# Optimization experiments

Measured on AMD Instinct MI355X. Metric: run time of the kernel, lower is better.

Reference implementation:

```python
import jax, jax.numpy as jnp
import numpy as np

D = 1024
H = 16
HD = D // H
L = 2048
B = 1
MLP = 8192
ROPE_BASE = 10000.0
LN_EPS = 1e-5


def layer_norm(x):
    mu = jnp.mean(x, axis=-1, keepdims=True)
    var = jnp.var(x, axis=-1, keepdims=True)
    return (x - mu) / jnp.sqrt(var + LN_EPS)


def rope(x):
    # x: [B, H, L, HD]; non-traditional (rotate-half / NeoX style)
    half = HD // 2
    inv_freq = 1.0 / (ROPE_BASE ** (jnp.arange(0, half, dtype=jnp.float32) / half))
    pos = jnp.arange(x.shape[2], dtype=jnp.float32)
    ang = pos[:, None] * inv_freq[None, :]            # [L, half]
    cos, sin = jnp.cos(ang), jnp.sin(ang)
    x1, x2 = x[..., :half], x[..., half:]
    return jnp.concatenate([x1 * cos - x2 * sin, x2 * cos + x1 * sin], axis=-1).astype(x.dtype)


def setup_inputs() -> dict:
    key = jax.random.key(0)
    ks = jax.random.split(key, 5)
    x = jax.random.normal(ks[0], (B, L, D), dtype=jnp.float32)
    # causal additive mask
    neg = jnp.finfo(jnp.float32).min
    mask = jnp.where(jnp.tril(jnp.ones((L, L), dtype=bool)), 0.0, neg).astype(jnp.float32)
    W_attn = jax.random.normal(ks[1], (3 * D, D), dtype=jnp.float32) * (D ** -0.5)
    W_out = jax.random.normal(ks[2], (D, D), dtype=jnp.float32) * (D ** -0.5)
    W_ffp = jax.random.normal(ks[3], (MLP, D), dtype=jnp.float32) * (D ** -0.5)
    W_ffo = jax.random.normal(ks[4], (D, MLP // 2), dtype=jnp.float32) * ((MLP // 2) ** -0.5)
    return {"x": x, "mask": mask, "W_attn": W_attn, "W_out": W_out, "W_ffp": W_ffp, "W_ffo": W_ffo}


def block(x, mask, W_attn, W_out, W_ffp, W_ffo):
    b, l, d = x.shape
    scale = HD ** -0.5
    # attention branch
    xn = layer_norm(x)
    qkv = xn @ W_attn.T                                    # [B, L, 3D]
    q, k, v = jnp.split(qkv, 3, axis=-1)
    q = q.reshape(b, l, H, HD).transpose(0, 2, 1, 3)       # [B, H, L, HD]
    k = k.reshape(b, l, H, HD).transpose(0, 2, 1, 3)
    v = v.reshape(b, l, H, HD).transpose(0, 2, 1, 3)
    q = rope(q)
    k = rope(k)
    scores = jnp.einsum('bhqd,bhkd->bhqk', q * scale, k)   # [B, H, L, L]
    scores = scores + mask
    probs = jax.nn.softmax(scores.astype(jnp.float32), axis=-1).astype(scores.dtype)
    attn = jnp.einsum('bhqk,bhkd->bhqd', probs, v)
    attn = attn.transpose(0, 2, 1, 3).reshape(b, l, d)
    r = attn @ W_out.T
    h = x + r
    # SwiGLU MLP branch: split ff_proj output, swiglu(x2, x1) = silu(x2) * x1
    g = layer_norm(h) @ W_ffp.T                            # [B, L, MLP]
    x1, x2 = jnp.split(g, 2, axis=-1)
    mlp = (jax.nn.silu(x2) * x1) @ W_ffo.T
    return h + mlp


def reference(x, mask, W_attn, W_out, W_ffp, W_ffo):
    return block(x, mask, W_attn, W_out, W_ffp, W_ffo)
```

## Files before the change

### kernel.cpp

```cpp
#include <hip/hip_runtime.h>
#include <math.h>

#define DMODEL 1024
#define NHEAD  16
#define HDIM   64
#define SEQ    2048
#define MLPD   8192
#define HALF_MLP 4096
static constexpr float LN_EPS_C = 1e-5f;
#define NEG_BIG (-1e30f)
#define SM_SHIFT 16.0f

typedef short bf16x8 __attribute__((ext_vector_type(8)));
typedef float f32x4  __attribute__((ext_vector_type(4)));

__device__ __forceinline__ unsigned short f2b(float f) {
    unsigned int u = __float_as_uint(f);
    u = (u + 0x7FFFu + ((u >> 16) & 1u)) >> 16;
    return (unsigned short)u;
}
__device__ __forceinline__ float b2f(unsigned short h) {
    return __uint_as_float((unsigned int)h << 16);
}

__device__ __forceinline__ void async_copy16(const unsigned short* g, unsigned short* l) {
    __builtin_amdgcn_global_load_lds(
        (const __attribute__((address_space(1))) unsigned int*)(g),
        (__attribute__((address_space(3))) unsigned int*)(l),
        16, 0, 0);
}

__global__ void prep_all(const float* __restrict__ x,
                         const float* __restrict__ W_attn, const float* __restrict__ W_out,
                         const float* __restrict__ W_ffp,  const float* __restrict__ W_ffo,
                         unsigned short* __restrict__ xnb, float2* __restrict__ ct,
                         unsigned short* __restrict__ oa, unsigned short* __restrict__ ob,
                         unsigned short* __restrict__ oc, unsigned short* __restrict__ od) {
    const int bid = blockIdx.x;
    const int tid = threadIdx.x;
    if (bid < SEQ) {
        __shared__ float rs[256], rs2[256];
        float4 v = *(const float4*)(x + (size_t)bid * DMODEL + tid * 4);
        rs[tid]  = v.x + v.y + v.z + v.w;
        rs2[tid] = v.x * v.x + v.y * v.y + v.z * v.z + v.w * v.w;
        __syncthreads();
        for (int off = 128; off > 0; off >>= 1) {
            if (tid < off) { rs[tid] += rs[tid + off]; rs2[tid] += rs2[tid + off]; }
            __syncthreads();
        }
        float mu  = rs[0] * (1.0f / DMODEL);
        float var = rs2[0] * (1.0f / DMODEL) - mu * mu;
        float inv = rsqrtf(var + LN_EPS_C);
        ushort4 o;
        o.x = f2b((v.x - mu) * inv); o.y = f2b((v.y - mu) * inv);
        o.z = f2b((v.z - mu) * inv); o.w = f2b((v.w - mu) * inv);
        *(ushort4*)(xnb + (size_t)bid * DMODEL + tid * 4) = o;
    } else if (bid < SEQ + 256) {
        int idx = (bid - SEQ) * 256 + tid;
        int pos = idx >> 5, p = idx & 31;
        float invf = powf(10000.0f, -(float)p / 32.0f);
        float ang = (float)pos * invf;
        ct[idx] = make_float2(cosf(ang), sinf(ang));
    } else {
        const int n1 = 3 * DMODEL * DMODEL;
        const int n2 = n1 + DMODEL * DMODEL;
        const int n3 = n2 + MLPD * DMODEL;
        int i = ((bid - SEQ - 256) * 256 + tid) * 4;
        const float* src; unsigned short* dst; int off;
        if (i < n1)      { src = W_attn; dst = oa; off = i; }
        else if (i < n2) { src = W_out;  dst = ob; off = i - n1; }
        else if (i < n3) {
            src = W_ffp; off = i - n2;
            int row = off >> 10, col = off & 1023;
            int rp  = (row < HALF_MLP) ? (2 * row) : (2 * (row - HALF_MLP) + 1);
            float4 v = *(const float4*)(src + off);
            ushort4 o;
            o.x = f2b(v.x); o.y = f2b(v.y); o.z = f2b(v.z); o.w = f2b(v.w);
            *(ushort4*)(oc + ((size_t)rp << 10) + col) = o;
            return;
        }
        else             { src = W_ffo; dst = od; off = i - n3; }
        float4 v = *(const float4*)(src + off);
        ushort4 o;
        o.x = f2b(v.x); o.y = f2b(v.y); o.z = f2b(v.z); o.w = f2b(v.w);
        *(ushort4*)(dst + off) = o;
    }
}

__global__ void ln_red2(const float* __restrict__ p0, const float* __restrict__ p1,
                        const float* __restrict__ x, float* __restrict__ h,
                        unsigned short* __restrict__ xnb) {
    const int row = blockIdx.x;
    const int tid = threadIdx.x;
    __shared__ float rs[256], rs2[256];
    const size_t base = (size_t)row * DMODEL + tid * 4;
    float4 a = *(const float4*)(p0 + base);
    float4 b = *(const float4*)(p1 + base);
    float4 r = *(const float4*)(x + base);
    float4 v = { a.x + b.x + r.x, a.y + b.y + r.y, a.z + b.z + r.z, a.w + b.w + r.w };
    *(float4*)(h + base) = v;
    rs[tid]  = v.x + v.y + v.z + v.w;
    rs2[tid] = v.x * v.x + v.y * v.y + v.z * v.z + v.w * v.w;
    __syncthreads();
    for (int off = 128; off > 0; off >>= 1) {
        if (tid < off) { rs[tid] += rs[tid + off]; rs2[tid] += rs2[tid + off]; }
        __syncthreads();
    }
    float mu  = rs[0] * (1.0f / DMODEL);
    float var = rs2[0] * (1.0f / DMODEL) - mu * mu;
    float inv = rsqrtf(var + LN_EPS_C);
    ushort4 o;
    o.x = f2b((v.x - mu) * inv); o.y = f2b((v.y - mu) * inv);
    o.z = f2b((v.z - mu) * inv); o.w = f2b((v.w - mu) * inv);
    *(ushort4*)(xnb + base) = o;
}

__global__ __launch_bounds__(256)
void gemm_qkv(const unsigned short* __restrict__ A, const unsigned short* __restrict__ B,
              const float2* __restrict__ ct,
              unsigned short* __restrict__ Qp, unsigned short* __restrict__ Kp,
              unsigned short* __restrict__ Vt) {
    __shared__ unsigned short As[128 * 32];
    __shared__ unsigned short Bs[128 * 32];
    __shared__ unsigned short St[4][16][72];
    const int tid  = threadIdx.x;
    const int lane = tid & 63;
    const int w    = tid >> 6;
    const int wm   = w >> 1;
    const int wn   = w & 1;
    const int m0   = blockIdx.y * 128;
    const int n0   = blockIdx.x * 128;

    f32x4 acc[4][4] = {};

    const int srow = lane >> 2;
    const int scol = (lane & 3) * 8;
    const unsigned short* Abase = A + (size_t)(m0 + w * 32 + srow) * DMODEL + scol;
    const unsigned short* Bbase = B + (size_t)(n0 + w * 32 + srow) * DMODEL + scol;
    unsigned short* AsW = &As[(w * 32) * 32];
    unsigned short* BsW = &Bs[(w * 32) * 32];

    const int fr = lane & 15;
    const int fk = (lane >> 4) * 8;

    for (int k0 = 0; k0 < DMODEL; k0 += 32) {
        async_copy16(Abase + k0,               AsW);
        async_copy16(Abase + k0 + 16 * DMODEL, AsW + 16 * 32);
        async_copy16(Bbase + k0,               BsW);
        async_copy16(Bbase + k0 + 16 * DMODEL, BsW + 16 * 32);
        __syncthreads();

        bf16x8 af[4], bfr[4];
#pragma unroll
        for (int i = 0; i < 4; ++i)
            af[i] = *(const bf16x8*)(&As[(wm * 64 + i * 16 + fr) * 32 + fk]);
#pragma unroll
        for (int j = 0; j < 4; ++j)
            bfr[j] = *(const bf16x8*)(&Bs[(wn * 64 + j * 16 + fr) * 32 + fk]);
#pragma unroll
        for (int i = 0; i < 4; ++i)
#pragma unroll
            for (int j = 0; j < 4; ++j)
                acc[i][j] = __builtin_amdgcn_mfma_f32_16x16x32_bf16(af[i], bfr[j], acc[i][j], 0, 0, 0);
        __syncthreads();
    }

    const int erow   = (lane >> 4) * 4;
    const int ecol   = lane & 15;
    const int region = blockIdx.x >> 3;
    const int head   = ((n0 + wn * 64) >> 6) & 15;

    if (region == 2) {
        const int sbase = m0 + wm * 64;
        const int dl = lane >> 3;
        const int ch = (lane & 7) * 8;
#pragma unroll
        for (int j = 0; j < 4; ++j) {
#pragma unroll
            for (int i = 0; i < 4; ++i) {
                ushort4 o;
                o.x = f2b(acc[i][j][0]); o.y = f2b(acc[i][j][1]);
                o.z = f2b(acc[i][j][2]); o.w = f2b(acc[i][j][3]);
                *(ushort4*)&St[w][ecol][i * 16 + erow] = o;
            }
#pragma unroll
            for (int p = 0; p < 2; ++p) {
                const int dd = p * 8 + dl;
                bf16x8 v = *(const bf16x8*)&St[w][dd][ch];
                *(bf16x8*)(Vt + ((size_t)head * HDIM + j * 16 + dd) * SEQ + sbase + ch) = v;
            }
        }
    } else {
        unsigned short* P = region ? Kp : Qp;
        const float scale = region ? 1.0f : 0.125f;
        unsigned short* qb = &St[w][erow][0];
#pragma unroll
        for (int i = 0; i < 4; ++i) {
#pragma unroll
            for (int r = 0; r < 4; ++r) {
                const int rowg = m0 + wm * 64 + i * 16 + erow + r;
                const float2* crow = ct + (size_t)rowg * 32;
#pragma unroll
                for (int jj = 0; jj < 2; ++jj) {
                    const float2 cs = crow[jj * 16 + ecol];
                    const float x1 = acc[i][jj][r];
                    const float x2 = acc[i][jj + 2][r];
                    qb[jj * 16 + ecol]      = f2b((x1 * cs.x - x2 * cs.y) * scale);
                    qb[jj * 16 + ecol + 32] = f2b((x2 * cs.x + x1 * cs.y) * scale);
                }
                ushort4 o = *(const ushort4*)&qb[ecol * 4];
                *(ushort4*)(P + ((size_t)head * SEQ + rowg) * HDIM + ecol * 4) = o;
            }
        }
    }
}

__global__ __launch_bounds__(256)
void gemm_mfma_sk(const unsigned short* __restrict__ A, const unsigned short* __restrict__ B,
                  float* __restrict__ P, int Ksub, int lda, int ldb, int ldc) {
    __shared__ unsigned short As[128 * 32];
    __shared__ unsigned short Bs[128 * 32];
    const int tid  = threadIdx.x;
    const int lane = tid & 63;
    const int w    = tid >> 6;
    const int wm   = w >> 1;
    const int wn   = w & 1;
    const int m0   = blockIdx.y * 128;
    const int n0   = blockIdx.x * 128;
    const int kb   = blockIdx.z * Ksub;

    f32x4 acc[4][4] = {};

    const int srow = lane >> 2;
    const int scol = (lane & 3) * 8;
    const unsigned short* Abase = A + (size_t)(m0 + w * 32 + srow) * lda + scol + kb;
    const unsigned short* Bbase = B + (size_t)(n0 + w * 32 + srow) * ldb + scol + kb;
    unsigned short* AsW = &As[(w * 32) * 32];
    unsigned short* BsW = &Bs[(w * 32) * 32];

    const int fr = lane & 15;
    const int fk = (lane >> 4) * 8;

    for (int k0 = 0; k0 < Ksub; k0 += 32) {
        async_copy16(Abase + k0,            AsW);
        async_copy16(Abase + k0 + 16 * lda, AsW + 16 * 32);
        async_copy16(Bbase + k0,            BsW);
        async_copy16(Bbase + k0 + 16 * (size_t)ldb, BsW + 16 * 32);
        __syncthreads();

        bf16x8 af[4], bfr[4];
#pragma unroll
        for (int i = 0; i < 4; ++i)
            af[i] = *(const bf16x8*)(&As[(wm * 64 + i * 16 + fr) * 32 + fk]);
#pragma unroll
        for (int j = 0; j < 4; ++j)
            bfr[j] = *(const bf16x8*)(&Bs[(wn * 64 + j * 16 + fr) * 32 + fk]);
#pragma unroll
        for (int i = 0; i < 4; ++i)
#pragma unroll
            for (int j = 0; j < 4; ++j)
                acc[i][j] = __builtin_amdgcn_mfma_f32_16x16x32_bf16(af[i], bfr[j], acc[i][j], 0, 0, 0);
        __syncthreads();
    }

    float* Pp = P + (size_t)blockIdx.z * SEQ * ldc;
    const int erow = (lane >> 4) * 4;
    const int ecol = lane & 15;
#pragma unroll
    for (int i = 0; i < 4; ++i)
#pragma unroll
        for (int j = 0; j < 4; ++j) {
            const int colg = n0 + wn * 64 + j * 16 + ecol;
#pragma unroll
            for (int r = 0; r < 4; ++r) {
                const int rowg = m0 + wm * 64 + i * 16 + erow + r;
                Pp[(size_t)rowg * ldc + colg] = acc[i][j][r];
            }
        }
}

__global__ void reduce4_kernel(const float* __restrict__ p0, const float* __restrict__ p1,
                               const float* __restrict__ p2, const float* __restrict__ p3,
                               const float* __restrict__ res, float* __restrict__ out) {
    int i = (blockIdx.x * blockDim.x + threadIdx.x) * 4;
    float4 a = *(const float4*)(p0 + i);
    float4 b = *(const float4*)(p1 + i);
    float4 c = *(const float4*)(p2 + i);
    float4 d = *(const float4*)(p3 + i);
    float4 r = *(const float4*)(res + i);
    float4 o = { a.x + b.x + c.x + d.x + r.x, a.y + b.y + c.y + d.y + r.y,
                 a.z + b.z + c.z + d.z + r.z, a.w + b.w + c.w + d.w + r.w };
    *(float4*)(out + i) = o;
}

#define STW 40
__global__ __launch_bounds__(256)
void gemm_ffp_silu(const unsigned short* __restrict__ A, const unsigned short* __restrict__ B,
                   unsigned short* __restrict__ gact) {
    __shared__ unsigned short As[128 * 32];
    __shared__ unsigned short Bs[128 * 32];
    __shared__ unsigned short St[4][64][STW];
    const int tid  = threadIdx.x;
    const int lane = tid & 63;
    const int w    = tid >> 6;
    const int wm   = w >> 1;
    const int wn   = w & 1;
    const int m0   = blockIdx.y * 128;
    const int n0   = blockIdx.x * 128;

    f32x4 acc[4][4] = {};

    const int srow = lane >> 2;
    const int scol = (lane & 3) * 8;
    const unsigned short* Abase = A + (size_t)(m0 + w * 32 + srow) * DMODEL + scol;
    const unsigned short* Bbase = B + (size_t)(n0 + w * 32 + srow) * DMODEL + scol;
    unsigned short* AsW = &As[(w * 32) * 32];
    unsigned short* BsW = &Bs[(w * 32) * 32];

    const int fr = lane & 15;
    const int fk = (lane >> 4) * 8;

    for (int k0 = 0; k0 < DMODEL; k0 += 32) {
        async_copy16(Abase + k0,               AsW);
        async_copy16(Abase + k0 + 16 * DMODEL, AsW + 16 * 32);
        async_copy16(Bbase + k0,               BsW);
        async_copy16(Bbase + k0 + 16 * DMODEL, BsW + 16 * 32);
        __syncthreads();

        bf16x8 af[4], bfr[4];
#pragma unroll
        for (int i = 0; i < 4; ++i)
            af[i] = *(const bf16x8*)(&As[(wm * 64 + i * 16 + fr) * 32 + fk]);
#pragma unroll
        for (int j = 0; j < 4; ++j)
            bfr[j] = *(const bf16x8*)(&Bs[(wn * 64 + j * 16 + fr) * 32 + fk]);
#pragma unroll
        for (int i = 0; i < 4; ++i)
#pragma unroll
            for (int j = 0; j < 4; ++j)
                acc[i][j] = __builtin_amdgcn_mfma_f32_16x16x32_bf16(af[i], bfr[j], acc[i][j], 0, 0, 0);
        __syncthreads();
    }

    const int erow = (lane >> 4) * 4;
    const int ecol = lane & 15;
    const bool evn = (ecol & 1) == 0;
#pragma unroll
    for (int i = 0; i < 4; ++i)
#pragma unroll
        for (int j = 0; j < 4; ++j)
#pragma unroll
            for (int r = 0; r < 4; ++r) {
                float own = acc[i][j][r];
                float oth = __shfl_xor(own, 1);
                if (evn) {
                    float sil = oth / (1.0f + __expf(-oth));
                    St[w][i * 16 + erow + r][j * 8 + (ecol >> 1)] = f2b(sil * own);
                }
            }
    {
        const int rowg = m0 + wm * 64 + lane;
        unsigned short* dst = gact + (size_t)rowg * HALF_MLP + (n0 >> 1) + wn * 32;
        bf16x8 v0 = *(const bf16x8*)&St[w][lane][0];
        bf16x8 v1 = *(const bf16x8*)&St[w][lane][8];
        bf16x8 v2 = *(const bf16x8*)&St[w][lane][16];
        bf16x8 v3 = *(const bf16x8*)&St[w][lane][24];
        *(bf16x8*)(dst + 0)  = v0;
        *(bf16x8*)(dst + 8)  = v1;
        *(bf16x8*)(dst + 16) = v2;
        *(bf16x8*)(dst + 24) = v3;
    }
}

__global__ __launch_bounds__(256)
void fattn_blk(const unsigned short* __restrict__ Qp,
               const unsigned short* __restrict__ Kp,
               const unsigned short* __restrict__ Vt,
               unsigned short* __restrict__ out) {
    __shared__ unsigned short Ks[2][64][64];
    __shared__ unsigned short Vs[2][64][64];
    __shared__ unsigned short Ps[4][16][72];
    const int tid  = threadIdx.x;
    const int lane = tid & 63;
    const int w    = tid >> 6;
    const int fr   = lane & 15;
    const int quad = lane >> 4;

    const int f    = blockIdx.x;
    const int head = ((f & 7) << 1) | ((f >> 3) & 1);
    const int ub   = f >> 4;
    const int qb   = (ub & 1) ? (31 - (ub >> 1)) : (ub >> 1);
    const int m0   = qb * 64 + w * 16;

    const unsigned short* Qg = Qp + (size_t)head * SEQ * HDIM;
    const unsigned short* Kg = Kp + (size_t)head * SEQ * HDIM;
    const unsigned short* Vg = Vt + (size_t)head * HDIM * SEQ;

    const int rA = (w << 3) + (lane >> 3);
    const int cg = ((lane & 7) ^ ((lane >> 3) & 7)) << 3;

    bf16x8 qf[2];
#pragma unroll
    for (int kk = 0; kk < 2; ++kk)
        qf[kk] = *(const bf16x8*)(Qg + (size_t)(m0 + fr) * HDIM + kk * 32 + quad * 8);

    bf16x8 ones;
#pragma unroll
    for (int e = 0; e < 8; ++e) ones[e] = (short)0x3F80;

    f32x4 accO[4] = {};
    f32x4 accL = {};

    const int ntiles = qb + 1;

    {
        const unsigned short* gk = Kg + (size_t)rA * HDIM + cg;
        unsigned short* dk = &Ks[0][w << 3][0];
        async_copy16(gk, dk);
        async_copy16(gk + 32 * HDIM, dk + 32 * 64);
        const unsigned short* gv = Vg + (size_t)rA * SEQ + cg;
        unsigned short* dv = &Vs[0][w << 3][0];
        async_copy16(gv, dv);
        async_copy16(gv + 32 * SEQ, dv + 32 * 64);
    }
    __syncthreads();

    int cur = 0;
    for (int t = 0; t < ntiles; ++t) {
        if (t + 1 < ntiles) {
            const int j1 = (t + 1) * 64;
            const unsigned short* gk = Kg + (size_t)(j1 + rA) * HDIM + cg;
            unsigned short* dk = &Ks[cur ^ 1][w << 3][0];
            async_copy16(gk, dk);
            async_copy16(gk + 32 * HDIM, dk + 32 * 64);
            const unsigned short* gv = Vg + (size_t)rA * SEQ + j1 + cg;
            unsigned short* dv = &Vs[cur ^ 1][w << 3][0];
            async_copy16(gv, dv);
            async_copy16(gv + 32 * SEQ, dv + 32 * 64);
        }

        const int j0 = t * 64;
        f32x4 accS[4] = {};
#pragma unroll
        for (int kk = 0; kk < 2; ++kk) {
#pragma unroll
            for (int j = 0; j < 4; ++j) {
                bf16x8 kf = *(const bf16x8*)
                    &Ks[cur][j * 16 + fr][(((kk << 2) + quad) ^ (fr & 7)) << 3];
                accS[j] = __builtin_amdgcn_mfma_f32_16x16x32_bf16(qf[kk], kf, accS[j], 0, 0, 0);
            }
        }

        if (t == ntiles - 1) {
#pragma unroll
            for (int j = 0; j < 4; ++j)
#pragma unroll
                for (int r = 0; r < 4; ++r)
                    if (j0 + j * 16 + fr > m0 + quad * 4 + r) accS[j][r] = NEG_BIG;
        }

#pragma unroll
        for (int j = 0; j < 4; ++j)
#pragma unroll
            for (int r = 0; r < 4; ++r)
                Ps[w][quad * 4 + r][j * 16 + fr] = f2b(__expf(accS[j][r] - SM_SHIFT));

#pragma unroll
        for (int kk = 0; kk < 2; ++kk) {
            bf16x8 pf = *(const bf16x8*)&Ps[w][fr][kk * 32 + quad * 8];
            accL = __builtin_amdgcn_mfma_f32_16x16x32_bf16(pf, ones, accL, 0, 0, 0);
#pragma unroll
            for (int j = 0; j < 4; ++j) {
                bf16x8 vf = *(const bf16x8*)
                    &Vs[cur][j * 16 + fr][(((kk << 2) + quad) ^ (fr & 7)) << 3];
                accO[j] = __builtin_amdgcn_mfma_f32_16x16x32_bf16(pf, vf, accO[j], 0, 0, 0);
            }
        }

        __syncthreads();
        cur ^= 1;
    }

#pragma unroll
    for (int r = 0; r < 4; ++r) {
        const float inv = 1.0f / accL[r];
        const int qrow = m0 + quad * 4 + r;
#pragma unroll
        for (int j = 0; j < 4; ++j)
            out[(size_t)qrow * DMODEL + head * HDIM + j * 16 + fr] = f2b(accO[j][r] * inv);
    }
}

extern "C" void kernel_launch(void* const* d_in, const int* in_sizes, int n_in,
                              void* d_out, int out_size, void* d_ws, size_t ws_size,
                              hipStream_t stream) {
    const float* x      = (const float*)d_in[0];
    const float* W_attn = (const float*)d_in[2];
    const float* W_out  = (const float*)d_in[3];
    const float* W_ffp  = (const float*)d_in[4];
    const float* W_ffo  = (const float*)d_in[5];
    float* out = (float*)d_out;

    char* wsb = (char*)d_ws;
    unsigned short* wb_attn = (unsigned short*)(wsb);
    unsigned short* wb_out  = (unsigned short*)(wsb + (6u  << 20));
    unsigned short* wb_ffp  = (unsigned short*)(wsb + (8u  << 20));
    unsigned short* wb_ffo  = (unsigned short*)(wsb + (24u << 20));
    float*          h       = (float*)(wsb + (32u << 20));
    unsigned short* xnb     = (unsigned short*)(wsb + (40u << 20));
    unsigned short* attnb   = (unsigned short*)(wsb + (44u << 20));
    unsigned short* gact    = (unsigned short*)(wsb + (48u << 20));
    unsigned short* Qp      = (unsigned short*)(wsb + (64u << 20));
    unsigned short* Kp      = (unsigned short*)(wsb + (68u << 20));
    unsigned short* Vt      = (unsigned short*)(wsb + (72u << 20));
    float*          wout_p  = (float*)(wsb + (76u << 20));
    float2*         ct      = (float2*)(wsb + (92u << 20));
    float*          ffo_p   = (float*)(wsb + (64u << 20));

    {
        int f2b_blocks = (3 * DMODEL * DMODEL + DMODEL * DMODEL + MLPD * DMODEL
                          + DMODEL * HALF_MLP) / 4 / 256;
        prep_all<<<SEQ + 256 + f2b_blocks, 256, 0, stream>>>(
            x, W_attn, W_out, W_ffp, W_ffo, xnb, ct,
            wb_attn, wb_out, wb_ffp, wb_ffo);
    }

    gemm_qkv<<<dim3(3 * DMODEL / 128, SEQ / 128), 256, 0, stream>>>(
        xnb, wb_attn, ct, Qp, Kp, Vt);

    fattn_blk<<<512, 256, 0, stream>>>(Qp, Kp, Vt, attnb);

    gemm_mfma_sk<<<dim3(DMODEL / 128, SEQ / 128, 2), 256, 0, stream>>>(
        attnb, wb_out, wout_p, DMODEL / 2, DMODEL, DMODEL, DMODEL);

    ln_red2<<<SEQ, 256, 0, stream>>>(wout_p, wout_p + (size_t)SEQ * DMODEL, x, h, xnb);

    gemm_ffp_silu<<<dim3(MLPD / 128, SEQ / 128), 256, 0, stream>>>(
        xnb, wb_ffp, gact);

    gemm_mfma_sk<<<dim3(DMODEL / 128, SEQ / 128, 4), 256, 0, stream>>>(
        gact, wb_ffo, ffo_p, HALF_MLP / 4, HALF_MLP, HALF_MLP, DMODEL);

    reduce4_kernel<<<SEQ * DMODEL / 4 / 256, 256, 0, stream>>>(
        ffo_p, ffo_p + (size_t)SEQ * DMODEL, ffo_p + 2 * (size_t)SEQ * DMODEL,
        ffo_p + 3 * (size_t)SEQ * DMODEL, h, out);
}
```

Before: 310.9 us.

## Rewrite FFP SwiGLU GEMM with 256x256 tiles and multi-stage async pipeline

Replaces the 128x128, 256-thread FFP+SiLU GEMM with a 512-thread kernel computing 256x256 output tiles. Global-to-LDS copies rotate through four buffers, prefetching two k-steps ahead, with explicit vmcnt waits and a single barrier per iteration. It also adds an XOR swizzle on LDS chunks to avoid bank conflicts, a block-index remap for L2 locality, and raised wave priority around the MFMA loop. The aim is to hide load latency and raise arithmetic intensity, at the cost of 128KB of LDS per block and higher register pressure from the larger accumulator, which limits occupancy.

```diff
diff --git a/kernel.cpp b/kernel.cpp
--- a/kernel.cpp
+++ b/kernel.cpp
@@ -293,60 +293,93 @@
     *(float4*)(out + i) = o;
 }
 
-#define STW 40
-__global__ __launch_bounds__(256)
-void gemm_ffp_silu(const unsigned short* __restrict__ A, const unsigned short* __restrict__ B,
-                   unsigned short* __restrict__ gact) {
-    __shared__ unsigned short As[128 * 32];
-    __shared__ unsigned short Bs[128 * 32];
-    __shared__ unsigned short St[4][64][STW];
+#define FT  32
+#define FNT (DMODEL / FT)
+__global__ __launch_bounds__(512, 2)
+void gemm_ffp_silu_p(const unsigned short* __restrict__ A,
+                     const unsigned short* __restrict__ B,
+                     unsigned short* __restrict__ gact) {
+    __shared__ __align__(16) unsigned short U[4][2][256 * 32];
     const int tid  = threadIdx.x;
     const int lane = tid & 63;
     const int w    = tid >> 6;
-    const int wm   = w >> 1;
-    const int wn   = w & 1;
-    const int m0   = blockIdx.y * 128;
-    const int n0   = blockIdx.x * 128;
-
-    f32x4 acc[4][4] = {};
-
-    const int srow = lane >> 2;
-    const int scol = (lane & 3) * 8;
-    const unsigned short* Abase = A + (size_t)(m0 + w * 32 + srow) * DMODEL + scol;
-    const unsigned short* Bbase = B + (size_t)(n0 + w * 32 + srow) * DMODEL + scol;
-    unsigned short* AsW = &As[(w * 32) * 32];
-    unsigned short* BsW = &Bs[(w * 32) * 32];
-
-    const int fr = lane & 15;
-    const int fk = (lane >> 4) * 8;
-
-    for (int k0 = 0; k0 < DMODEL; k0 += 32) {
-        async_copy16(Abase + k0,               AsW);
-        async_copy16(Abase + k0 + 16 * DMODEL, AsW + 16 * 32);
-        async_copy16(Bbase + k0,               BsW);
-        async_copy16(Bbase + k0 + 16 * DMODEL, BsW + 16 * 32);
-        __syncthreads();
-
-        bf16x8 af[4], bfr[4];
-#pragma unroll
-        for (int i = 0; i < 4; ++i)
-            af[i] = *(const bf16x8*)(&As[(wm * 64 + i * 16 + fr) * 32 + fk]);
+    const int wm   = w >> 2;
+    const int wn   = w & 3;
+    const int fr   = lane & 15;
+    const int quad = lane >> 4;
+
+    const int sid = (blockIdx.x & 7) * 32 + (blockIdx.x >> 3);
+    const int tm  = sid & 7;
+    const int tn  = sid >> 3;
+
+    const unsigned short* Ag = A + (size_t)(tm * 256) * DMODEL;
+    const unsigned short* Bg = B + (size_t)(tn * 256) * DMODEL;
+
+    const int srow = tid >> 2;
+    const int scg  = ((tid & 3) ^ ((tid >> 3) & 3)) * 8;
+    unsigned short* lba = (unsigned short*)&U[0][0][0] + w * 512;
+    unsigned short* lbb = (unsigned short*)&U[0][1][0] + w * 512;
+
+    const int rchunk = (quad ^ ((fr >> 1) & 3)) * 8;
+
+    f32x4 acc[8][4] = {};
+
+#define FFP_STAGE(T)                                                          \
+    {                                                                         \
+        const int k0_ = (T) * FT;                                             \
+        const int sl_ = (T) & 3;                                              \
+        const unsigned short* ga_ = Ag + (size_t)srow * DMODEL + k0_ + scg;   \
+        const unsigned short* gb_ = Bg + (size_t)srow * DMODEL + k0_ + scg;   \
+        unsigned short* la_ = lba + sl_ * 16384;                              \
+        unsigned short* lb_ = lbb + sl_ * 16384;                              \
+        async_copy16(ga_,                la_);                                \
+        async_copy16(ga_ + 128 * DMODEL, la_ + 4096);                         \
+        async_copy16(gb_,                lb_);                                \
+        async_copy16(gb_ + 128 * DMODEL, lb_ + 4096);                         \
+    }
+
+    FFP_STAGE(0)
+    FFP_STAGE(1)
+
+    for (int t = 0; t < FNT; ++t) {
+        if (t + 2 < FNT) {
+            FFP_STAGE(t + 2)
+            asm volatile("s_waitcnt vmcnt(8)" ::: "memory");
+        } else if (t + 1 < FNT) {
+            asm volatile("s_waitcnt vmcnt(4)" ::: "memory");
+        } else {
+            asm volatile("s_waitcnt vmcnt(0)" ::: "memory");
+        }
+        __builtin_amdgcn_s_barrier();
+        __builtin_amdgcn_sched_barrier(0);
+
+        const unsigned short* As_ = &U[t & 3][0][0];
+        const unsigned short* Bs_ = &U[t & 3][1][0];
+        bf16x8 af[8], bf[4];
+#pragma unroll
+        for (int i = 0; i < 8; ++i)
+            af[i] = *(const bf16x8*)&As_[(wm * 128 + i * 16 + fr) * 32 + rchunk];
 #pragma unroll
         for (int j = 0; j < 4; ++j)
-            bfr[j] = *(const bf16x8*)(&Bs[(wn * 64 + j * 16 + fr) * 32 + fk]);
-#pragma unroll
-        for (int i = 0; i < 4; ++i)
+            bf[j] = *(const bf16x8*)&Bs_[(wn * 64 + j * 16 + fr) * 32 + rchunk];
+
+        __builtin_amdgcn_s_setprio(1);
+#pragma unroll
+        for (int i = 0; i < 8; ++i)
 #pragma unroll
             for (int j = 0; j < 4; ++j)
-                acc[i][j] = __builtin_amdgcn_mfma_f32_16x16x32_bf16(af[i], bfr[j], acc[i][j], 0, 0, 0);
-        __syncthreads();
-    }
-
-    const int erow = (lane >> 4) * 4;
-    const int ecol = lane & 15;
-    const bool evn = (ecol & 1) == 0;
-#pragma unroll
-    for (int i = 0; i < 4; ++i)
+                acc[i][j] = __builtin_amdgcn_mfma_f32_16x16x32_bf16(af[i], bf[j], acc[i][j], 0, 0, 0);
+        __builtin_amdgcn_s_setprio(0);
+    }
+#undef FFP_STAGE
+
+    __syncthreads();
+    typedef unsigned short StRow[40];
+    StRow* Stw = reinterpret_cast<StRow*>(&U[0][0][0]) + (size_t)w * 128;
+
+    const bool evn = (fr & 1) == 0;
+#pragma unroll
+    for (int i = 0; i < 8; ++i)
 #pragma unroll
         for (int j = 0; j < 4; ++j)
 #pragma unroll
@@ -355,20 +388,25 @@
                 float oth = __shfl_xor(own, 1);
                 if (evn) {
                     float sil = oth / (1.0f + __expf(-oth));
-                    St[w][i * 16 + erow + r][j * 8 + (ecol >> 1)] = f2b(sil * own);
+                    Stw[i * 16 + quad * 4 + r][j * 8 + (fr >> 1)] = f2b(sil * own);
                 }
             }
     {
-        const int rowg = m0 + wm * 64 + lane;
-        unsigned short* dst = gact + (size_t)rowg * HALF_MLP + (n0 >> 1) + wn * 32;
-        bf16x8 v0 = *(const bf16x8*)&St[w][lane][0];
-        bf16x8 v1 = *(const bf16x8*)&St[w][lane][8];
-        bf16x8 v2 = *(const bf16x8*)&St[w][lane][16];
-        bf16x8 v3 = *(const bf16x8*)&St[w][lane][24];
-        *(bf16x8*)(dst + 0)  = v0;
-        *(bf16x8*)(dst + 8)  = v1;
-        *(bf16x8*)(dst + 16) = v2;
-        *(bf16x8*)(dst + 24) = v3;
+        const int growb = tm * 256 + wm * 128;
+        const int colb  = tn * 128 + wn * 32;
+#pragma unroll
+        for (int p = 0; p < 2; ++p) {
+            const int rl = p * 64 + lane;
+            unsigned short* dst = gact + (size_t)(growb + rl) * HALF_MLP + colb;
+            bf16x8 v0 = *(const bf16x8*)&Stw[rl][0];
+            bf16x8 v1 = *(const bf16x8*)&Stw[rl][8];
+            bf16x8 v2 = *(const bf16x8*)&Stw[rl][16];
+            bf16x8 v3 = *(const bf16x8*)&Stw[rl][24];
+            *(bf16x8*)(dst + 0)  = v0;
+            *(bf16x8*)(dst + 8)  = v1;
+            *(bf16x8*)(dst + 16) = v2;
+            *(bf16x8*)(dst + 24) = v3;
+        }
     }
 }
 
@@ -535,8 +573,7 @@
 
     ln_red2<<<SEQ, 256, 0, stream>>>(wout_p, wout_p + (size_t)SEQ * DMODEL, x, h, xnb);
 
-    gemm_ffp_silu<<<dim3(MLPD / 128, SEQ / 128), 256, 0, stream>>>(
-        xnb, wb_ffp, gact);
+    gemm_ffp_silu_p<<<256, 512, 0, stream>>>(xnb, wb_ffp, gact);
 
     gemm_mfma_sk<<<dim3(DMODEL / 128, SEQ / 128, 4), 256, 0, stream>>>(
         gact, wb_ffo, ffo_p, HALF_MLP / 4, HALF_MLP, HALF_MLP, DMODEL);
```

After: 297.8 us. -4.2%, faster.
